# Performance work log

Measured on AMD Instinct MI355X. Metric: run time of the kernel, lower is better.

Reference implementation:

```python
import jax, jax.numpy as jnp
import numpy as np

N_NODES = 10000
N_EDGES = 80000
F_NODE = 16
F_EDGE = 8
BN_EPS = 1e-5


def _nnconv(x, src, dst, edge_attr, w1, b1, w2, b2, w_root, bias, cin, cout):
    # edge MLP -> per-edge weight matrices [E, cin, cout]
    h = jax.nn.relu(edge_attr @ w1 + b1) @ w2 + b2
    w = h.reshape(-1, cin, cout)
    # gather source node features, per-edge matmul
    msg = jnp.einsum('ei,eio->eo', x[src], w)  # [E, cout]
    # scatter-mean into target nodes
    deg = jax.ops.segment_sum(jnp.ones(msg.shape[0], x.dtype), dst, num_segments=N_NODES)
    agg = jax.ops.segment_sum(msg, dst, num_segments=N_NODES) / jnp.clip(deg, 1.0)[:, None]
    return x @ w_root + agg + bias


def _batchnorm(x, gamma, beta):
    m = jnp.mean(x, axis=0)
    v = jnp.mean((x - m) ** 2, axis=0)  # biased var, as torch BN training mode
    return (x - m) * jax.lax.rsqrt(v + BN_EPS) * gamma + beta


def setup_inputs() -> dict:
    key = jax.random.key(0)
    ks = jax.random.split(key, 24)
    s = 0.05
    inp = {
        'x': jax.random.normal(ks[0], (N_NODES, F_NODE), jnp.float32),
        'edge_index': jax.random.randint(ks[1], (2, N_EDGES), 0, N_NODES, jnp.int32),
        'edge_attr': jax.random.normal(ks[2], (N_EDGES, F_EDGE), jnp.float32),
        # conv1 edge MLP: F_EDGE -> 25 -> 32*F_NODE
        'nn1_w1': jax.random.normal(ks[3], (F_EDGE, 25), jnp.float32) * s,
        'nn1_b1': jnp.zeros((25,), jnp.float32),
        'nn1_w2': jax.random.normal(ks[4], (25, 32 * F_NODE), jnp.float32) * s,
        'nn1_b2': jnp.zeros((32 * F_NODE,), jnp.float32),
        'conv1_root': jax.random.normal(ks[5], (F_NODE, 32), jnp.float32) * s,
        'conv1_bias': jnp.zeros((32,), jnp.float32),
        'bn1_gamma': jnp.ones((32,), jnp.float32),
        'bn1_beta': jnp.zeros((32,), jnp.float32),
        # conv2 edge MLP: F_EDGE -> 25 -> 32*64
        'nn2_w1': jax.random.normal(ks[6], (F_EDGE, 25), jnp.float32) * s,
        'nn2_b1': jnp.zeros((25,), jnp.float32),
        'nn2_w2': jax.random.normal(ks[7], (25, 32 * 64), jnp.float32) * s,
        'nn2_b2': jnp.zeros((32 * 64,), jnp.float32),
        'conv2_root': jax.random.normal(ks[8], (32, 64), jnp.float32) * s,
        'conv2_bias': jnp.zeros((64,), jnp.float32),
        'bn2_gamma': jnp.ones((64,), jnp.float32),
        'bn2_beta': jnp.zeros((64,), jnp.float32),
        'fc1_w': jax.random.normal(ks[9], (64, 128), jnp.float32) * s,
        'fc1_b': jnp.zeros((128,), jnp.float32),
        'fc2_w': jax.random.normal(ks[10], (128, 1), jnp.float32) * s,
        'fc2_b': jnp.zeros((1,), jnp.float32),
    }
    return inp


def reference(x, edge_index, edge_attr,
              nn1_w1, nn1_b1, nn1_w2, nn1_b2, conv1_root, conv1_bias, bn1_gamma, bn1_beta,
              nn2_w1, nn2_b1, nn2_w2, nn2_b2, conv2_root, conv2_bias, bn2_gamma, bn2_beta,
              fc1_w, fc1_b, fc2_w, fc2_b):
    src, dst = edge_index[0], edge_index[1]
    h = jax.nn.elu(_nnconv(x, src, dst, edge_attr, nn1_w1, nn1_b1, nn1_w2, nn1_b2,
                           conv1_root, conv1_bias, F_NODE, 32))
    h = jax.nn.elu(_batchnorm(h, bn1_gamma, bn1_beta))
    h = jax.nn.elu(_nnconv(h, src, dst, edge_attr, nn2_w1, nn2_b1, nn2_w2, nn2_b2,
                           conv2_root, conv2_bias, 32, 64))
    h = jax.nn.elu(_batchnorm(h, bn2_gamma, bn2_beta))
    h = jax.nn.elu(h @ fc1_w + fc1_b)
    h = jax.nn.elu(h @ fc2_w + fc2_b)  # [N, 1]
    # single graph: sum over all nodes -> shape [1]
    return jnp.sum(h).reshape(1)
```

## Files before the change

### kernel.cpp

```cpp
#include <hip/hip_runtime.h>
#include <hip/hip_bf16.h>
#include <hip/hip_fp16.h>

#define N_NODES 10000
#define N_EDGES 80000
#define FN 16
#define FE 8
#define HID 25
#define C1 32
#define C2 64
#define NU_BLOCKS 256
#define FC_BLOCKS 640
#define HROW 28
#define SLOTS 40
#define SC_BLOCKS ((N_EDGES + 255) / 256)
#define TN 25

typedef _Float16 h16;
typedef _Float16 h16x4 __attribute__((ext_vector_type(4)));

__device__ __forceinline__ float elu_f(float x) { return x > 0.f ? x : (expf(x) - 1.f); }

__device__ __forceinline__ float hdot(const h16* __restrict__ row, const float* Pk) {
    const h16x4* rv = (const h16x4*)row;
    float s = 0.f;
#pragma unroll
    for (int q = 0; q < 7; q++) {
        h16x4 hv = rv[q];
        s += (float)hv.x * Pk[4 * q] + (float)hv.y * Pk[4 * q + 1] +
             (float)hv.z * Pk[4 * q + 2] + (float)hv.w * Pk[4 * q + 3];
    }
    return s;
}

template <int CIN, int COUT>
__device__ __forceinline__ void pre_block(const float* __restrict__ xin,
                                          const float* __restrict__ w2,
                                          const float* __restrict__ b2,
                                          h16* __restrict__ P, int u, int tid) {
    constexpr int M = (HID + 1) * COUT;
    constexpr int MB = (M + 255) / 256;
    int mb = u % MB;
    int n0 = (u / MB) * TN;
    int m = mb * 256 + tid;
    if (m >= M) return;
    int k = m / COUT, o = m % COUT;
    float wreg[CIN];
    if (k < HID) {
#pragma unroll
        for (int i = 0; i < CIN; i++) wreg[i] = w2[(size_t)(k * CIN + i) * COUT + o];
    } else {
#pragma unroll
        for (int i = 0; i < CIN; i++) wreg[i] = b2[i * COUT + o];
    }
    for (int n = n0; n < n0 + TN; n++) {
        const float* xr = xin + (size_t)n * CIN;
        float s = 0.f;
#pragma unroll
        for (int i = 0; i < CIN; i++) s += xr[i] * wreg[i];
        P[(size_t)n * M + m] = (h16)s;
    }
}

__global__ void k_scatter_pre1(const float* __restrict__ ea, const int* __restrict__ ei,
                               const float* __restrict__ w1a, const float* __restrict__ b1a,
                               const float* __restrict__ w1b, const float* __restrict__ b1b,
                               const float* __restrict__ x, const float* __restrict__ w2a,
                               const float* __restrict__ b2a,
                               int* __restrict__ cnt_src, int* __restrict__ cnt_dst,
                               int* __restrict__ ebuf, h16* __restrict__ h1r,
                               h16* __restrict__ h2r, h16* __restrict__ P1) {
    int tid = threadIdx.x;
    int bid = blockIdx.x;
    if (bid >= SC_BLOCKS) {
        pre_block<FN, C1>(x, w2a, b2a, P1, bid - SC_BLOCKS, tid);
        return;
    }
    __shared__ float sw1a[FE * HID], sw1b[FE * HID], sb1a[HID], sb1b[HID];
    for (int i = tid; i < FE * HID; i += 256) { sw1a[i] = w1a[i]; sw1b[i] = w1b[i]; }
    if (tid < HID) { sb1a[tid] = b1a[tid]; sb1b[tid] = b1b[tid]; }
    __syncthreads();
    int e = bid * 256 + tid;
    if (e >= N_EDGES) return;
    float a[FE];
#pragma unroll
    for (int i = 0; i < FE; i++) a[i] = ea[e * FE + i];
    int src = ei[e], dst = ei[N_EDGES + e];
    int slot = atomicAdd(&cnt_src[src], 1);
    ebuf[src * SLOTS + slot] = (e << 14) | dst;
    atomicAdd(&cnt_dst[dst], 1);
    h16 b1buf[HROW], b2buf[HROW];
#pragma unroll
    for (int k = 0; k < HID; k++) {
        float s1 = sb1a[k], s2 = sb1b[k];
#pragma unroll
        for (int i = 0; i < FE; i++) { s1 += a[i] * sw1a[i * HID + k]; s2 += a[i] * sw1b[i * HID + k]; }
        b1buf[k] = (h16)fmaxf(s1, 0.f);
        b2buf[k] = (h16)fmaxf(s2, 0.f);
    }
    b1buf[25] = (h16)1.f; b1buf[26] = (h16)0.f; b1buf[27] = (h16)0.f;
    b2buf[25] = (h16)1.f; b2buf[26] = (h16)0.f; b2buf[27] = (h16)0.f;
    h16x4* h1p = (h16x4*)(h1r + (size_t)e * HROW);
    h16x4* h2p = (h16x4*)(h2r + (size_t)e * HROW);
#pragma unroll
    for (int q = 0; q < 7; q++) {
        h1p[q] = ((const h16x4*)b1buf)[q];
        h2p[q] = ((const h16x4*)b2buf)[q];
    }
}

template <int CIN, int COUT>
__global__ void k_precompute(const float* __restrict__ xin, const float* __restrict__ w2,
                             const float* __restrict__ b2, h16* __restrict__ P) {
    pre_block<CIN, COUT>(xin, w2, b2, P, blockIdx.x, threadIdx.x);
}

__global__ void k_msg_c1(const h16* __restrict__ P, const int* __restrict__ cnt_src,
                         const int* __restrict__ ebuf, const h16* __restrict__ h1r,
                         float* __restrict__ agg) {
    constexpr int M = (HID + 1) * C1;
    int lane = threadIdx.x & 63;
    int o = lane & 31;
    int n = __builtin_amdgcn_readfirstlane(blockIdx.x * 4 + (threadIdx.x >> 6));
    if (n >= N_NODES) return;
    const h16* Pr = P + (size_t)n * M;
    float Pk[HROW];
#pragma unroll
    for (int k = 0; k <= HID; k++) Pk[k] = (float)Pr[k * C1 + o];
    Pk[26] = 0.f; Pk[27] = 0.f;
    int beg = n * SLOTS, end = beg + cnt_src[n];
    int idx = beg;
    for (; idx + 3 < end; idx += 4) {
        int p0 = ebuf[idx], p1 = ebuf[idx + 1], p2 = ebuf[idx + 2], p3 = ebuf[idx + 3];
        float s0 = hdot(h1r + (size_t)(p0 >> 14) * HROW, Pk);
        float s1 = hdot(h1r + (size_t)(p1 >> 14) * HROW, Pk);
        float s2 = hdot(h1r + (size_t)(p2 >> 14) * HROW, Pk);
        float s3 = hdot(h1r + (size_t)(p3 >> 14) * HROW, Pk);
        float va = (lane < 32) ? s0 : s1;
        int da = (lane < 32) ? (p0 & 0x3FFF) : (p1 & 0x3FFF);
        atomicAdd(&agg[da * C1 + o], va);
        float vb = (lane < 32) ? s2 : s3;
        int db = (lane < 32) ? (p2 & 0x3FFF) : (p3 & 0x3FFF);
        atomicAdd(&agg[db * C1 + o], vb);
    }
    for (; idx + 1 < end; idx += 2) {
        int p0 = ebuf[idx], p1 = ebuf[idx + 1];
        float s0 = hdot(h1r + (size_t)(p0 >> 14) * HROW, Pk);
        float s1 = hdot(h1r + (size_t)(p1 >> 14) * HROW, Pk);
        float va = (lane < 32) ? s0 : s1;
        int da = (lane < 32) ? (p0 & 0x3FFF) : (p1 & 0x3FFF);
        atomicAdd(&agg[da * C1 + o], va);
    }
    if (idx < end) {
        int p0 = ebuf[idx];
        float s0 = hdot(h1r + (size_t)(p0 >> 14) * HROW, Pk);
        if (lane < 32) atomicAdd(&agg[(p0 & 0x3FFF) * C1 + o], s0);
    }
}

__global__ void k_msg_c2(const h16* __restrict__ P, const int* __restrict__ cnt_src,
                         const int* __restrict__ ebuf, const h16* __restrict__ h2r,
                         float* __restrict__ agg) {
    constexpr int M = (HID + 1) * C2;
    int lane = threadIdx.x & 63;
    int n = __builtin_amdgcn_readfirstlane(blockIdx.x * 4 + (threadIdx.x >> 6));
    if (n >= N_NODES) return;
    const h16* Pr = P + (size_t)n * M;
    float Pk[HROW];
#pragma unroll
    for (int k = 0; k <= HID; k++) Pk[k] = (float)Pr[k * C2 + lane];
    Pk[26] = 0.f; Pk[27] = 0.f;
    int beg = n * SLOTS, end = beg + cnt_src[n];
    int idx = beg;
    for (; idx + 3 < end; idx += 4) {
        int p0 = ebuf[idx], p1 = ebuf[idx + 1], p2 = ebuf[idx + 2], p3 = ebuf[idx + 3];
        float s0 = hdot(h2r + (size_t)(p0 >> 14) * HROW, Pk);
        float s1 = hdot(h2r + (size_t)(p1 >> 14) * HROW, Pk);
        float s2 = hdot(h2r + (size_t)(p2 >> 14) * HROW, Pk);
        float s3 = hdot(h2r + (size_t)(p3 >> 14) * HROW, Pk);
        atomicAdd(&agg[(p0 & 0x3FFF) * C2 + lane], s0);
        atomicAdd(&agg[(p1 & 0x3FFF) * C2 + lane], s1);
        atomicAdd(&agg[(p2 & 0x3FFF) * C2 + lane], s2);
        atomicAdd(&agg[(p3 & 0x3FFF) * C2 + lane], s3);
    }
    for (; idx < end; idx++) {
        int p0 = ebuf[idx];
        float s0 = hdot(h2r + (size_t)(p0 >> 14) * HROW, Pk);
        atomicAdd(&agg[(p0 & 0x3FFF) * C2 + lane], s0);
    }
}

template <int CIN, int COUT>
__global__ void k_node_update(const float* __restrict__ xin, const float* __restrict__ root,
                              const float* __restrict__ bias, const float* __restrict__ agg,
                              const int* __restrict__ degi, float* __restrict__ act,
                              float* __restrict__ s1g, float* __restrict__ s2g,
                              float* zero_out) {
    __shared__ float l1[256], l2[256];
    int tid = threadIdx.x;
    if (zero_out && blockIdx.x == 0 && tid == 0) *zero_out = 0.f;
    int o = tid % COUT;
    float b = bias[o];
    float rcol[CIN];
#pragma unroll
    for (int i = 0; i < CIN; i++) rcol[i] = root[i * COUT + o];
    float acc1 = 0.f, acc2 = 0.f;
    for (int t = blockIdx.x * 256 + tid; t < N_NODES * COUT; t += NU_BLOCKS * 256) {
        int n = t / COUT;
        const float* xr = xin + (size_t)n * CIN;
        float s = b;
#pragma unroll
        for (int i = 0; i < CIN; i++) s += xr[i] * rcol[i];
        s += agg[t] / fmaxf((float)degi[n], 1.0f);
        float a = elu_f(s);
        act[t] = a;
        acc1 += a; acc2 += a * a;
    }
    l1[tid] = acc1; l2[tid] = acc2;
    __syncthreads();
    for (int s = 128; s >= COUT; s >>= 1) {
        if (tid < s) { l1[tid] += l1[tid + s]; l2[tid] += l2[tid + s]; }
        __syncthreads();
    }
    if (tid < COUT) { atomicAdd(&s1g[tid], l1[tid]); atomicAdd(&s2g[tid], l2[tid]); }
}

template <int COUT>
__global__ void k_bn_elu(const float* __restrict__ act, const float* __restrict__ s1g,
                         const float* __restrict__ s2g, const float* __restrict__ gamma,
                         const float* __restrict__ beta, float* __restrict__ out) {
    int t = blockIdx.x * blockDim.x + threadIdx.x;
    if (t >= N_NODES * COUT) return;
    int o = t % COUT;
    float m = s1g[o] * (1.0f / N_NODES);
    float v = s2g[o] * (1.0f / N_NODES) - m * m;
    float x = (act[t] - m) * rsqrtf(v + 1e-5f) * gamma[o] + beta[o];
    out[t] = elu_f(x);
}

__global__ void k_fc_sum(const float* __restrict__ a2,
                         const float* __restrict__ s1g, const float* __restrict__ s2g,
                         const float* __restrict__ gamma, const float* __restrict__ beta,
                         const float* __restrict__ fc1w, const float* __restrict__ fc1b,
                         const float* __restrict__ fc2w, const float* __restrict__ fc2b,
                         float* __restrict__ out) {
    int tid = threadIdx.x;
    int lane = tid & 63;
    int wave = tid >> 6;
    float m = s1g[lane] * (1.0f / N_NODES);
    float var = s2g[lane] * (1.0f / N_NODES) - m * m;
    float scale = rsqrtf(var + 1e-5f) * gamma[lane];
    float shift = beta[lane] - m * scale;
    float b0 = fc1b[lane], b1 = fc1b[lane + 64];
    float w0 = fc2w[lane], w1 = fc2w[lane + 64];
    float fb = fc2b[0];
    float acc = 0.f;
    for (int n = blockIdx.x * 4 + wave; n < N_NODES; n += FC_BLOCKS * 4) {
        float hval = elu_f(a2[(size_t)n * C2 + lane] * scale + shift);
        float s0 = b0, s1 = b1;
#pragma unroll
        for (int i = 0; i < C2; i++) {
            float hv = __shfl(hval, i);
            s0 += hv * fc1w[i * 128 + lane];
            s1 += hv * fc1w[i * 128 + 64 + lane];
        }
        float v = elu_f(s0) * w0 + elu_f(s1) * w1;
#pragma unroll
        for (int off2 = 32; off2 > 0; off2 >>= 1) v += __shfl_down(v, off2);
        if (lane == 0) acc += elu_f(v + fb);
    }
    __shared__ float lds[4];
    if (lane == 0) lds[wave] = acc;
    __syncthreads();
    if (tid == 0) atomicAdd(out, lds[0] + lds[1] + lds[2] + lds[3]);
}

extern "C" void kernel_launch(void* const* d_in, const int* in_sizes, int n_in,
                              void* d_out, int out_size, void* d_ws, size_t ws_size,
                              hipStream_t stream) {
    const float* x       = (const float*)d_in[0];
    const int*   ei      = (const int*)d_in[1];
    const float* ea      = (const float*)d_in[2];
    const float* nn1_w1  = (const float*)d_in[3];
    const float* nn1_b1  = (const float*)d_in[4];
    const float* nn1_w2  = (const float*)d_in[5];
    const float* nn1_b2  = (const float*)d_in[6];
    const float* c1_root = (const float*)d_in[7];
    const float* c1_bias = (const float*)d_in[8];
    const float* bn1_g   = (const float*)d_in[9];
    const float* bn1_b   = (const float*)d_in[10];
    const float* nn2_w1  = (const float*)d_in[11];
    const float* nn2_b1  = (const float*)d_in[12];
    const float* nn2_w2  = (const float*)d_in[13];
    const float* nn2_b2  = (const float*)d_in[14];
    const float* c2_root = (const float*)d_in[15];
    const float* c2_bias = (const float*)d_in[16];
    const float* bn2_g   = (const float*)d_in[17];
    const float* bn2_b   = (const float*)d_in[18];
    const float* fc1_w   = (const float*)d_in[19];
    const float* fc1_b   = (const float*)d_in[20];
    const float* fc2_w   = (const float*)d_in[21];
    const float* fc2_b   = (const float*)d_in[22];
    float* out = (float*)d_out;

    char* ws = (char*)d_ws;
    size_t off = 0;
    auto alloc = [&](size_t nbytes) -> void* {
        void* q = (void*)(ws + off);
        off += nbytes;
        off = (off + 255) & ~(size_t)255;
        return q;
    };
    int*   cnt_src = (int*)alloc(N_NODES * 4);
    int*   cnt_dst = (int*)alloc(N_NODES * 4);
    float* agg1    = (float*)alloc((size_t)N_NODES * C1 * 4);
    float* agg2    = (float*)alloc((size_t)N_NODES * C2 * 4);
    float* bn1_s1  = (float*)alloc(C1 * 4);
    float* bn1_s2  = (float*)alloc(C1 * 4);
    float* bn2_s1  = (float*)alloc(C2 * 4);
    float* bn2_s2  = (float*)alloc(C2 * 4);
    size_t zero_bytes = off;
    int*   ebuf    = (int*)alloc((size_t)N_NODES * SLOTS * 4);
    h16*   h1r     = (h16*)alloc((size_t)N_EDGES * HROW * 2);
    h16*   h2r     = (h16*)alloc((size_t)N_EDGES * HROW * 2);
    h16*   P1      = (h16*)alloc((size_t)N_NODES * (HID + 1) * C1 * 2);
    h16*   P2      = (h16*)alloc((size_t)N_NODES * (HID + 1) * C2 * 2);
    float* a1      = (float*)alloc((size_t)N_NODES * C1 * 4);
    float* h1      = (float*)alloc((size_t)N_NODES * C1 * 4);
    float* a2      = (float*)alloc((size_t)N_NODES * C2 * 4);
    (void)ws_size; (void)in_sizes; (void)n_in; (void)out_size;

    hipMemsetAsync(d_ws, 0, zero_bytes, stream);

    constexpr int PRE1_BLOCKS = (((HID + 1) * C1 + 255) / 256) * (N_NODES / TN);
    constexpr int PRE2_BLOCKS = (((HID + 1) * C2 + 255) / 256) * (N_NODES / TN);

    k_scatter_pre1<<<SC_BLOCKS + PRE1_BLOCKS, 256, 0, stream>>>(
        ea, ei, nn1_w1, nn1_b1, nn2_w1, nn2_b1, x, nn1_w2, nn1_b2,
        cnt_src, cnt_dst, ebuf, h1r, h2r, P1);
    k_msg_c1<<<(N_NODES + 3) / 4, 256, 0, stream>>>(P1, cnt_src, ebuf, h1r, agg1);
    k_node_update<FN, C1><<<NU_BLOCKS, 256, 0, stream>>>(x, c1_root, c1_bias, agg1,
                                                         cnt_dst, a1, bn1_s1, bn1_s2, nullptr);
    k_bn_elu<C1><<<(N_NODES * C1) / 256, 256, 0, stream>>>(a1, bn1_s1, bn1_s2, bn1_g, bn1_b, h1);
    k_precompute<C1, C2><<<PRE2_BLOCKS, 256, 0, stream>>>(h1, nn2_w2, nn2_b2, P2);
    k_msg_c2<<<(N_NODES + 3) / 4, 256, 0, stream>>>(P2, cnt_src, ebuf, h2r, agg2);
    k_node_update<C1, C2><<<NU_BLOCKS, 256, 0, stream>>>(h1, c2_root, c2_bias, agg2,
                                                         cnt_dst, a2, bn2_s1, bn2_s2, out);
    k_fc_sum<<<FC_BLOCKS, 256, 0, stream>>>(a2, bn2_s1, bn2_s2, bn2_g, bn2_b,
                                            fc1_w, fc1_b, fc2_w, fc2_b, out);
}
```

Measured before the change: 244.3 us.

## Fuse per-node P precompute into message kernels via shared memory tiles

The per-node projection tables P1/P2 are no longer written to global memory in a separate pass. Each block now computes P for a tile of nodes into LDS and consumes it directly in the edge-message loop. The BN1+ELU pass is folded into the conv2 kernel's input staging, which also writes h1 for the later root update. This removes the global round-trip of the fp16 P buffers and two launches. The cost is heavy LDS use per block (about 53KB for conv2), which limits occupancy, and the weight loads are repeated in every tile.

```diff
diff --git a/kernel.cpp b/kernel.cpp
--- a/kernel.cpp
+++ b/kernel.cpp
@@ -1,5 +1,4 @@
 #include <hip/hip_runtime.h>
-#include <hip/hip_bf16.h>
 #include <hip/hip_fp16.h>
 
 #define N_NODES 10000
@@ -9,12 +8,15 @@
 #define HID 25
 #define C1 32
 #define C2 64
-#define NU_BLOCKS 256
-#define FC_BLOCKS 640
 #define HROW 28
 #define SLOTS 40
 #define SC_BLOCKS ((N_EDGES + 255) / 256)
-#define TN 25
+#define NU_BLOCKS 256
+#define FC_BLOCKS 640
+#define TB1 25
+#define TB2 16
+#define M1 ((HID + 1) * C1)
+#define M2 ((HID + 1) * C2)
 
 typedef _Float16 h16;
 typedef _Float16 h16x4 __attribute__((ext_vector_type(4)));
@@ -33,102 +35,10 @@
     return s;
 }
 
-template <int CIN, int COUT>
-__device__ __forceinline__ void pre_block(const float* __restrict__ xin,
-                                          const float* __restrict__ w2,
-                                          const float* __restrict__ b2,
-                                          h16* __restrict__ P, int u, int tid) {
-    constexpr int M = (HID + 1) * COUT;
-    constexpr int MB = (M + 255) / 256;
-    int mb = u % MB;
-    int n0 = (u / MB) * TN;
-    int m = mb * 256 + tid;
-    if (m >= M) return;
-    int k = m / COUT, o = m % COUT;
-    float wreg[CIN];
-    if (k < HID) {
-#pragma unroll
-        for (int i = 0; i < CIN; i++) wreg[i] = w2[(size_t)(k * CIN + i) * COUT + o];
-    } else {
-#pragma unroll
-        for (int i = 0; i < CIN; i++) wreg[i] = b2[i * COUT + o];
-    }
-    for (int n = n0; n < n0 + TN; n++) {
-        const float* xr = xin + (size_t)n * CIN;
-        float s = 0.f;
-#pragma unroll
-        for (int i = 0; i < CIN; i++) s += xr[i] * wreg[i];
-        P[(size_t)n * M + m] = (h16)s;
-    }
-}
-
-__global__ void k_scatter_pre1(const float* __restrict__ ea, const int* __restrict__ ei,
-                               const float* __restrict__ w1a, const float* __restrict__ b1a,
-                               const float* __restrict__ w1b, const float* __restrict__ b1b,
-                               const float* __restrict__ x, const float* __restrict__ w2a,
-                               const float* __restrict__ b2a,
-                               int* __restrict__ cnt_src, int* __restrict__ cnt_dst,
-                               int* __restrict__ ebuf, h16* __restrict__ h1r,
-                               h16* __restrict__ h2r, h16* __restrict__ P1) {
-    int tid = threadIdx.x;
-    int bid = blockIdx.x;
-    if (bid >= SC_BLOCKS) {
-        pre_block<FN, C1>(x, w2a, b2a, P1, bid - SC_BLOCKS, tid);
-        return;
-    }
-    __shared__ float sw1a[FE * HID], sw1b[FE * HID], sb1a[HID], sb1b[HID];
-    for (int i = tid; i < FE * HID; i += 256) { sw1a[i] = w1a[i]; sw1b[i] = w1b[i]; }
-    if (tid < HID) { sb1a[tid] = b1a[tid]; sb1b[tid] = b1b[tid]; }
-    __syncthreads();
-    int e = bid * 256 + tid;
-    if (e >= N_EDGES) return;
-    float a[FE];
-#pragma unroll
-    for (int i = 0; i < FE; i++) a[i] = ea[e * FE + i];
-    int src = ei[e], dst = ei[N_EDGES + e];
-    int slot = atomicAdd(&cnt_src[src], 1);
-    ebuf[src * SLOTS + slot] = (e << 14) | dst;
-    atomicAdd(&cnt_dst[dst], 1);
-    h16 b1buf[HROW], b2buf[HROW];
-#pragma unroll
-    for (int k = 0; k < HID; k++) {
-        float s1 = sb1a[k], s2 = sb1b[k];
-#pragma unroll
-        for (int i = 0; i < FE; i++) { s1 += a[i] * sw1a[i * HID + k]; s2 += a[i] * sw1b[i * HID + k]; }
-        b1buf[k] = (h16)fmaxf(s1, 0.f);
-        b2buf[k] = (h16)fmaxf(s2, 0.f);
-    }
-    b1buf[25] = (h16)1.f; b1buf[26] = (h16)0.f; b1buf[27] = (h16)0.f;
-    b2buf[25] = (h16)1.f; b2buf[26] = (h16)0.f; b2buf[27] = (h16)0.f;
-    h16x4* h1p = (h16x4*)(h1r + (size_t)e * HROW);
-    h16x4* h2p = (h16x4*)(h2r + (size_t)e * HROW);
-#pragma unroll
-    for (int q = 0; q < 7; q++) {
-        h1p[q] = ((const h16x4*)b1buf)[q];
-        h2p[q] = ((const h16x4*)b2buf)[q];
-    }
-}
-
-template <int CIN, int COUT>
-__global__ void k_precompute(const float* __restrict__ xin, const float* __restrict__ w2,
-                             const float* __restrict__ b2, h16* __restrict__ P) {
-    pre_block<CIN, COUT>(xin, w2, b2, P, blockIdx.x, threadIdx.x);
-}
-
-__global__ void k_msg_c1(const h16* __restrict__ P, const int* __restrict__ cnt_src,
-                         const int* __restrict__ ebuf, const h16* __restrict__ h1r,
-                         float* __restrict__ agg) {
-    constexpr int M = (HID + 1) * C1;
-    int lane = threadIdx.x & 63;
-    int o = lane & 31;
-    int n = __builtin_amdgcn_readfirstlane(blockIdx.x * 4 + (threadIdx.x >> 6));
-    if (n >= N_NODES) return;
-    const h16* Pr = P + (size_t)n * M;
-    float Pk[HROW];
-#pragma unroll
-    for (int k = 0; k <= HID; k++) Pk[k] = (float)Pr[k * C1 + o];
-    Pk[26] = 0.f; Pk[27] = 0.f;
-    int beg = n * SLOTS, end = beg + cnt_src[n];
+__device__ __forceinline__ void msg1_edges(const float* Pk, int beg, int end,
+                                           const int* __restrict__ ebuf,
+                                           const h16* __restrict__ h1r,
+                                           float* __restrict__ agg, int lane, int o) {
     int idx = beg;
     for (; idx + 3 < end; idx += 4) {
         int p0 = ebuf[idx], p1 = ebuf[idx + 1], p2 = ebuf[idx + 2], p3 = ebuf[idx + 3];
@@ -158,19 +68,10 @@
     }
 }
 
-__global__ void k_msg_c2(const h16* __restrict__ P, const int* __restrict__ cnt_src,
-                         const int* __restrict__ ebuf, const h16* __restrict__ h2r,
-                         float* __restrict__ agg) {
-    constexpr int M = (HID + 1) * C2;
-    int lane = threadIdx.x & 63;
-    int n = __builtin_amdgcn_readfirstlane(blockIdx.x * 4 + (threadIdx.x >> 6));
-    if (n >= N_NODES) return;
-    const h16* Pr = P + (size_t)n * M;
-    float Pk[HROW];
-#pragma unroll
-    for (int k = 0; k <= HID; k++) Pk[k] = (float)Pr[k * C2 + lane];
-    Pk[26] = 0.f; Pk[27] = 0.f;
-    int beg = n * SLOTS, end = beg + cnt_src[n];
+__device__ __forceinline__ void msg2_edges(const float* Pk, int beg, int end,
+                                           const int* __restrict__ ebuf,
+                                           const h16* __restrict__ h2r,
+                                           float* __restrict__ agg, int lane) {
     int idx = beg;
     for (; idx + 3 < end; idx += 4) {
         int p0 = ebuf[idx], p1 = ebuf[idx + 1], p2 = ebuf[idx + 2], p3 = ebuf[idx + 3];
@@ -190,6 +91,92 @@
     }
 }
 
+__global__ void k_scatter(const float* __restrict__ ea, const int* __restrict__ ei,
+                          const float* __restrict__ w1a, const float* __restrict__ b1a,
+                          const float* __restrict__ w1b, const float* __restrict__ b1b,
+                          int* __restrict__ cnt_src, int* __restrict__ cnt_dst,
+                          int* __restrict__ ebuf, h16* __restrict__ h1r,
+                          h16* __restrict__ h2r) {
+    int tid = threadIdx.x;
+    __shared__ float sw1a[FE * HID], sw1b[FE * HID], sb1a[HID], sb1b[HID];
+    for (int i = tid; i < FE * HID; i += 256) { sw1a[i] = w1a[i]; sw1b[i] = w1b[i]; }
+    if (tid < HID) { sb1a[tid] = b1a[tid]; sb1b[tid] = b1b[tid]; }
+    __syncthreads();
+    int e = blockIdx.x * 256 + tid;
+    if (e >= N_EDGES) return;
+    float a[FE];
+#pragma unroll
+    for (int i = 0; i < FE; i++) a[i] = ea[e * FE + i];
+    int src = ei[e], dst = ei[N_EDGES + e];
+    int slot = atomicAdd(&cnt_src[src], 1);
+    if (slot < SLOTS) ebuf[src * SLOTS + slot] = (e << 14) | dst;
+    atomicAdd(&cnt_dst[dst], 1);
+    h16 b1buf[HROW], b2buf[HROW];
+#pragma unroll
+    for (int k = 0; k < HID; k++) {
+        float s1 = sb1a[k], s2 = sb1b[k];
+#pragma unroll
+        for (int i = 0; i < FE; i++) { s1 += a[i] * sw1a[i * HID + k]; s2 += a[i] * sw1b[i * HID + k]; }
+        b1buf[k] = (h16)fmaxf(s1, 0.f);
+        b2buf[k] = (h16)fmaxf(s2, 0.f);
+    }
+    b1buf[25] = (h16)1.f; b1buf[26] = (h16)0.f; b1buf[27] = (h16)0.f;
+    b2buf[25] = (h16)1.f; b2buf[26] = (h16)0.f; b2buf[27] = (h16)0.f;
+    h16x4* h1p = (h16x4*)(h1r + (size_t)e * HROW);
+    h16x4* h2p = (h16x4*)(h2r + (size_t)e * HROW);
+#pragma unroll
+    for (int q = 0; q < 7; q++) {
+        h1p[q] = ((const h16x4*)b1buf)[q];
+        h2p[q] = ((const h16x4*)b2buf)[q];
+    }
+}
+
+__global__ __launch_bounds__(256, 3)
+void k_conv1(const float* __restrict__ x, const float* __restrict__ w2,
+             const float* __restrict__ b2, const int* __restrict__ cnt_src,
+             const int* __restrict__ ebuf, const h16* __restrict__ h1r,
+             float* __restrict__ agg) {
+    __shared__ h16 Pl[TB1 * M1];
+    __shared__ float xs[TB1 * FN];
+    int tid = threadIdx.x;
+    int n0 = blockIdx.x * TB1;
+    for (int t = tid; t < TB1 * FN; t += 256) xs[t] = x[(size_t)n0 * FN + t];
+    __syncthreads();
+#pragma unroll
+    for (int mm = 0; mm < 4; mm++) {
+        int m = mm * 256 + tid;
+        if (m < M1) {
+            int k = m >> 5, o = m & 31;
+            float wreg[FN];
+            if (k < HID) {
+#pragma unroll
+                for (int i = 0; i < FN; i++) wreg[i] = w2[(size_t)(k * FN + i) * C1 + o];
+            } else {
+#pragma unroll
+                for (int i = 0; i < FN; i++) wreg[i] = b2[i * C1 + o];
+            }
+            for (int n = 0; n < TB1; n++) {
+                float s = 0.f;
+#pragma unroll
+                for (int i = 0; i < FN; i++) s += xs[n * FN + i] * wreg[i];
+                Pl[n * M1 + m] = (h16)s;
+            }
+        }
+    }
+    __syncthreads();
+    int lane = tid & 63, wv = tid >> 6, o = lane & 31;
+    for (int dn = wv; dn < TB1; dn += 4) {
+        int n = n0 + dn;
+        float Pk[HROW];
+#pragma unroll
+        for (int k = 0; k <= HID; k++) Pk[k] = (float)Pl[dn * M1 + k * C1 + o];
+        Pk[26] = 0.f; Pk[27] = 0.f;
+        int deg = cnt_src[n];
+        deg = deg < SLOTS ? deg : SLOTS;
+        msg1_edges(Pk, n * SLOTS, n * SLOTS + deg, ebuf, h1r, agg, lane, o);
+    }
+}
+
 template <int CIN, int COUT>
 __global__ void k_node_update(const float* __restrict__ xin, const float* __restrict__ root,
                               const float* __restrict__ bias, const float* __restrict__ agg,
@@ -225,17 +212,61 @@
     if (tid < COUT) { atomicAdd(&s1g[tid], l1[tid]); atomicAdd(&s2g[tid], l2[tid]); }
 }
 
-template <int COUT>
-__global__ void k_bn_elu(const float* __restrict__ act, const float* __restrict__ s1g,
-                         const float* __restrict__ s2g, const float* __restrict__ gamma,
-                         const float* __restrict__ beta, float* __restrict__ out) {
-    int t = blockIdx.x * blockDim.x + threadIdx.x;
-    if (t >= N_NODES * COUT) return;
-    int o = t % COUT;
-    float m = s1g[o] * (1.0f / N_NODES);
-    float v = s2g[o] * (1.0f / N_NODES) - m * m;
-    float x = (act[t] - m) * rsqrtf(v + 1e-5f) * gamma[o] + beta[o];
-    out[t] = elu_f(x);
+__global__ __launch_bounds__(256, 2)
+void k_conv2(const float* __restrict__ a1, const float* __restrict__ s1g,
+             const float* __restrict__ s2g, const float* __restrict__ gamma,
+             const float* __restrict__ beta, const float* __restrict__ w2,
+             const float* __restrict__ b2, const int* __restrict__ cnt_src,
+             const int* __restrict__ ebuf, const h16* __restrict__ h2r,
+             float* __restrict__ agg, float* __restrict__ h1v) {
+    __shared__ h16 Pl[TB2 * M2];
+    __shared__ float xs[TB2 * C1];
+    int tid = threadIdx.x;
+    int n0 = blockIdx.x * TB2;
+    for (int t = tid; t < TB2 * C1; t += 256) {
+        int o = t & 31;
+        float m = s1g[o] * (1.0f / N_NODES);
+        float v = s2g[o] * (1.0f / N_NODES) - m * m;
+        float sc = rsqrtf(v + 1e-5f) * gamma[o];
+        float sh = beta[o] - m * sc;
+        float val = elu_f(a1[(size_t)n0 * C1 + t] * sc + sh);
+        xs[t] = val;
+        h1v[(size_t)n0 * C1 + t] = val;
+    }
+    __syncthreads();
+#pragma unroll
+    for (int mm = 0; mm < 7; mm++) {
+        int m = mm * 256 + tid;
+        if (m < M2) {
+            int k = m >> 6, o = m & 63;
+            float wreg[C1];
+            if (k < HID) {
+#pragma unroll
+                for (int i = 0; i < C1; i++) wreg[i] = w2[(size_t)(k * C1 + i) * C2 + o];
+            } else {
+#pragma unroll
+                for (int i = 0; i < C1; i++) wreg[i] = b2[i * C2 + o];
+            }
+            for (int n = 0; n < TB2; n++) {
+                float s = 0.f;
+#pragma unroll
+                for (int i = 0; i < C1; i++) s += xs[n * C1 + i] * wreg[i];
+                Pl[n * M2 + m] = (h16)s;
+            }
+        }
+    }
+    __syncthreads();
+    int lane = tid & 63, wv = tid >> 6;
+    for (int dn = wv; dn < TB2; dn += 4) {
+        int n = n0 + dn;
+        float Pk[HROW];
+#pragma unroll
+        for (int k = 0; k <= HID; k++) Pk[k] = (float)Pl[dn * M2 + k * C2 + lane];
+        Pk[26] = 0.f; Pk[27] = 0.f;
+        int deg = cnt_src[n];
+        deg = deg < SLOTS ? deg : SLOTS;
+        msg2_edges(Pk, n * SLOTS, n * SLOTS + deg, ebuf, h2r, agg, lane);
+    }
 }
 
 __global__ void k_fc_sum(const float* __restrict__ a2,
@@ -320,31 +351,24 @@
     float* bn2_s1  = (float*)alloc(C2 * 4);
     float* bn2_s2  = (float*)alloc(C2 * 4);
     size_t zero_bytes = off;
-    int*   ebuf    = (int*)alloc((size_t)N_NODES * SLOTS * 4);
-    h16*   h1r     = (h16*)alloc((size_t)N_EDGES * HROW * 2);
-    h16*   h2r     = (h16*)alloc((size_t)N_EDGES * HROW * 2);
-    h16*   P1      = (h16*)alloc((size_t)N_NODES * (HID + 1) * C1 * 2);
-    h16*   P2      = (h16*)alloc((size_t)N_NODES * (HID + 1) * C2 * 2);
-    float* a1      = (float*)alloc((size_t)N_NODES * C1 * 4);
-    float* h1      = (float*)alloc((size_t)N_NODES * C1 * 4);
-    float* a2      = (float*)alloc((size_t)N_NODES * C2 * 4);
+    int*   ebuf = (int*)alloc((size_t)N_NODES * SLOTS * 4);
+    h16*   h1r  = (h16*)alloc((size_t)N_EDGES * HROW * 2);
+    h16*   h2r  = (h16*)alloc((size_t)N_EDGES * HROW * 2);
+    float* a1   = (float*)alloc((size_t)N_NODES * C1 * 4);
+    float* h1v  = (float*)alloc((size_t)N_NODES * C1 * 4);
+    float* a2   = (float*)alloc((size_t)N_NODES * C2 * 4);
     (void)ws_size; (void)in_sizes; (void)n_in; (void)out_size;
 
     hipMemsetAsync(d_ws, 0, zero_bytes, stream);
 
-    constexpr int PRE1_BLOCKS = (((HID + 1) * C1 + 255) / 256) * (N_NODES / TN);
-    constexpr int PRE2_BLOCKS = (((HID + 1) * C2 + 255) / 256) * (N_NODES / TN);
-
-    k_scatter_pre1<<<SC_BLOCKS + PRE1_BLOCKS, 256, 0, stream>>>(
-        ea, ei, nn1_w1, nn1_b1, nn2_w1, nn2_b1, x, nn1_w2, nn1_b2,
-        cnt_src, cnt_dst, ebuf, h1r, h2r, P1);
-    k_msg_c1<<<(N_NODES + 3) / 4, 256, 0, stream>>>(P1, cnt_src, ebuf, h1r, agg1);
+    k_scatter<<<SC_BLOCKS, 256, 0, stream>>>(ea, ei, nn1_w1, nn1_b1, nn2_w1, nn2_b1,
+                                             cnt_src, cnt_dst, ebuf, h1r, h2r);
+    k_conv1<<<N_NODES / TB1, 256, 0, stream>>>(x, nn1_w2, nn1_b2, cnt_src, ebuf, h1r, agg1);
     k_node_update<FN, C1><<<NU_BLOCKS, 256, 0, stream>>>(x, c1_root, c1_bias, agg1,
                                                          cnt_dst, a1, bn1_s1, bn1_s2, nullptr);
-    k_bn_elu<C1><<<(N_NODES * C1) / 256, 256, 0, stream>>>(a1, bn1_s1, bn1_s2, bn1_g, bn1_b, h1);
-    k_precompute<C1, C2><<<PRE2_BLOCKS, 256, 0, stream>>>(h1, nn2_w2, nn2_b2, P2);
-    k_msg_c2<<<(N_NODES + 3) / 4, 256, 0, stream>>>(P2, cnt_src, ebuf, h2r, agg2);
-    k_node_update<C1, C2><<<NU_BLOCKS, 256, 0, stream>>>(h1, c2_root, c2_bias, agg2,
+    k_conv2<<<N_NODES / TB2, 256, 0, stream>>>(a1, bn1_s1, bn1_s2, bn1_g, bn1_b,
+                                               nn2_w2, nn2_b2, cnt_src, ebuf, h2r, agg2, h1v);
+    k_node_update<C1, C2><<<NU_BLOCKS, 256, 0, stream>>>(h1v, c2_root, c2_bias, agg2,
                                                          cnt_dst, a2, bn2_s1, bn2_s2, out);
     k_fc_sum<<<FC_BLOCKS, 256, 0, stream>>>(a2, bn2_s1, bn2_s2, bn2_g, bn2_b,
                                             fc1_w, fc1_b, fc2_w, fc2_b, out);
```

Measured after the change: 303.3 us. 1.24x slower.
